# Kernel optimization log

Hardware: AMD Instinct MI355X
Metric: run time of the kernel (lower is better)

Reference implementation:

```python
import jax, jax.numpy as jnp
import numpy as np

B, S, L, Q = 128, 200, 50, 20   # batch, story sentences, sentence len, query len
V, D, K = 50000, 128, 3          # vocab, embed dim, n_hops


def _pe(J, d):
    # position encoding l_kj = (1 - j/J) - (k/d)(1 - 2j/J), 1-indexed
    j = jnp.arange(1, J + 1, dtype=jnp.float32)[:, None]
    k = jnp.arange(1, d + 1, dtype=jnp.float32)[None, :]
    return 1.0 - j / J - (k / d) * (1.0 - 2.0 * j / J)  # (J, d)


def setup_inputs() -> dict:
    key = jax.random.key(0)
    ks = jax.random.split(key, 5)
    story = jax.random.randint(ks[0], (B, S, L), 0, V)
    query = jax.random.randint(ks[1], (B, Q), 0, V)
    # K+1 embedding tables (adjacent weight sharing: A^{k+1} = C^k), sigma=0.1, padding row 0 zeroed
    embs = (jax.random.normal(ks[2], (K + 1, V, D)) * 0.1).at[:, 0, :].set(0.0)
    TA = jax.random.normal(ks[3], (K, S, D)) * 0.1
    TC = jax.random.normal(ks[4], (K, S, D)) * 0.1
    return {"story": story, "query": query, "embs": embs, "TA": TA, "TC": TC}


def reference(story, query, embs, TA, TC):
    d = embs.shape[-1]
    pe_s = _pe(story.shape[-1], d)   # (L, D)
    pe_q = _pe(query.shape[-1], d)   # (Q, D)
    n_hops = TA.shape[0]

    # query embedding with PE: (B, Q, D) * (Q, D) -> sum over Q -> (B, D)
    u = (jnp.take(embs[0], query, axis=0) * pe_q).sum(axis=1)

    for hop in range(n_hops):
        # gather + PE multiply + sum over words + temporal encoding: (B, S, D)
        m = (jnp.take(embs[hop], story, axis=0) * pe_s).sum(axis=2) + TA[hop]
        c = (jnp.take(embs[hop + 1], story, axis=0) * pe_s).sum(axis=2) + TC[hop]
        # attention over memory slots
        p = jax.nn.softmax(jnp.einsum('bsd,bd->bs', m, u), axis=-1)  # (B, S)
        o = jnp.einsum('bs,bsd->bd', p, c)                            # (B, D)
        u = u + o

    # final projection W = embeddings[n_hops].weight -> logits (B, V)
    return u @ embs[n_hops].T
```

## Files before the change

### kernel.cpp

```cpp
#include <hip/hip_runtime.h>

#define B 128
#define S 200
#define LW 50
#define Q 20
#define V 50000
#define D 128
#define NH 3
#define VD (V * D)
#define BSD (B * S * D)
#define BS (B * S)

typedef __bf16 bf16x8 __attribute__((ext_vector_type(8)));
typedef float f32x4 __attribute__((ext_vector_type(4)));
typedef unsigned int u32x4 __attribute__((ext_vector_type(4)));

__device__ __forceinline__ unsigned int f2bf_rne(float f) {
  union { float f; unsigned int u; } c; c.f = f;
  return (c.u + 0x7FFFu + ((c.u >> 16) & 1u)) >> 16;
}
__device__ __forceinline__ unsigned int pack2(float a, float b) {
  return f2bf_rne(a) | (f2bf_rne(b) << 16);
}
__device__ __forceinline__ float bf_lo(unsigned int q) {
  union { unsigned int u; float f; } c; c.u = q << 16; return c.f;
}
__device__ __forceinline__ float bf_hi(unsigned int q) {
  union { unsigned int u; float f; } c; c.u = q & 0xFFFF0000u; return c.f;
}

__global__ __launch_bounds__(256) void k_repack(
    const float* __restrict__ embs, unsigned int* __restrict__ ESM) {
  int v = blockIdx.x * 4 + (threadIdx.x >> 6);
  int l = threadIdx.x & 63;
  int s = l >> 4, c = l & 15;
#pragma unroll
  for (int k = 0; k < 4; ++k) {
    const float2 e = *(const float2*)(embs + (size_t)k * VD + (size_t)v * D + 2 * l);
    ESM[((size_t)(k * 4 + s) * V + v) * 16 + c] = pack2(e.x, e.y);
  }
}

__global__ __launch_bounds__(256) void k_story16(
    const int* __restrict__ story, unsigned short* __restrict__ story16) {
  int i = blockIdx.x * 256 + threadIdx.x;
  int4 v = ((const int4*)story)[i];
  ushort4 o;
  o.x = (unsigned short)v.x; o.y = (unsigned short)v.y;
  o.z = (unsigned short)v.z; o.w = (unsigned short)v.w;
  ((ushort4*)story16)[i] = o;
}

__global__ __launch_bounds__(256) void k_packT(
    const float* __restrict__ TA, const float* __restrict__ TC,
    unsigned int* __restrict__ TAp, unsigned int* __restrict__ TCp) {
  int idx = blockIdx.x * 256 + threadIdx.x;
  int row = idx >> 6;
  int u = idx & 63;
  int d0 = 32 * (u >> 4) + 2 * (u & 15);
  const float2 a = *(const float2*)(TA + (size_t)row * D + d0);
  const float2 c = *(const float2*)(TC + (size_t)row * D + d0);
  TAp[idx] = pack2(a.x, a.y);
  TCp[idx] = pack2(c.x, c.y);
}

__global__ __launch_bounds__(256) void k_gather_slice(
    const unsigned short* __restrict__ story16,
    const u32x4* __restrict__ ESM4, unsigned int* __restrict__ Gp, int phase) {
  __shared__ __align__(16) unsigned short sidx[4][800];
  int unit = blockIdx.x & 7;
  int k = 2 * phase + (unit >> 2);
  int s = unit & 3;
  int widx = blockIdx.x >> 3;
  int w = threadIdx.x >> 6;
  int l = threadIdx.x & 63;
  int g = l >> 2;
  int q = l & 3;
  const u32x4* src4 = ESM4 + (size_t)(k * 4 + s) * V * 4;
  int d0 = s * 32 + 8 * q;
  float kd[8];
#pragma unroll
  for (int i = 0; i < 8; ++i) kd[i] = (float)(d0 + i + 1) * (1.0f / D);

  int sent16 = widx * 64 + w * 16;
  const u32x4* st4 = (const u32x4*)(story16 + sent16 * LW);
  u32x4* dst4 = (u32x4*)sidx[w];
#pragma unroll
  for (int m = 0; m < 2; ++m) {
    int e = l + m * 64;
    if (e < 100) dst4[e] = __builtin_nontemporal_load(st4 + e);
  }
  const unsigned short* wrow = sidx[w] + g * LW;
  float SA[8] = {0.f, 0.f, 0.f, 0.f, 0.f, 0.f, 0.f, 0.f};
  float SB[8] = {0.f, 0.f, 0.f, 0.f, 0.f, 0.f, 0.f, 0.f};
#pragma unroll 10
  for (int j = 0; j < LW; ++j) {
    int idx = (int)wrow[j];
    u32x4 qv = src4[(size_t)idx * 4 + q];
    float jj = (float)(j + 1) * (1.0f / LW);
    float al = 1.0f - jj;
    float bl = 2.0f * jj - 1.0f;
    float ee[8];
    ee[0] = bf_lo(qv.x); ee[1] = bf_hi(qv.x);
    ee[2] = bf_lo(qv.y); ee[3] = bf_hi(qv.y);
    ee[4] = bf_lo(qv.z); ee[5] = bf_hi(qv.z);
    ee[6] = bf_lo(qv.w); ee[7] = bf_hi(qv.w);
#pragma unroll
    for (int i = 0; i < 8; ++i) { SA[i] += ee[i] * al; SB[i] += ee[i] * bl; }
  }
  int sent = sent16 + g;
  u32x4 og;
  og.x = pack2(SA[0] + kd[0] * SB[0], SA[1] + kd[1] * SB[1]);
  og.y = pack2(SA[2] + kd[2] * SB[2], SA[3] + kd[3] * SB[3]);
  og.z = pack2(SA[4] + kd[4] * SB[4], SA[5] + kd[5] * SB[5]);
  og.w = pack2(SA[6] + kd[6] * SB[6], SA[7] + kd[7] * SB[7]);
  __builtin_nontemporal_store(
      og, (u32x4*)(Gp + ((size_t)k * BS + sent) * 64 + s * 16) + q);
}

__global__ __launch_bounds__(1024) void k_hops(
    const unsigned int* __restrict__ G, const unsigned int* __restrict__ TAp,
    const unsigned int* __restrict__ TCp, const int* __restrict__ query,
    const float* __restrict__ emb0, unsigned int* __restrict__ ubf) {
  __shared__ float su[D];
  __shared__ float sp[S];
  __shared__ float sred[2];
  __shared__ float4 oacc[32][32];
  int b = blockIdx.x;
  int t = threadIdx.x;
  if (t < D) {
    float kd = (float)(t + 1) * (1.0f / D);
    float acc = 0.f;
    for (int q = 0; q < Q; ++q) {
      int idx = query[b * Q + q];
      float jj = (float)(q + 1) * (1.0f / Q);
      float pe = 1.0f - jj - kd * (1.0f - 2.0f * jj);
      acc += emb0[(size_t)idx * D + t] * pe;
    }
    su[t] = acc;
  }
  __syncthreads();
  for (int hop = 0; hop < NH; ++hop) {
    const unsigned int* Gm = G + ((size_t)hop * BS + (size_t)b * S) * 64;
    const unsigned int* Gc = G + ((size_t)(hop + 1) * BS + (size_t)b * S) * 64;
    const unsigned int* ta = TAp + (size_t)hop * S * 64;
    const unsigned int* tc = TCp + (size_t)hop * S * 64;
    if (t < 4 * S) {
      int sl = t >> 2, p = t & 3;
      const uint2* gr = (const uint2*)(Gm + (size_t)sl * 64 + p * 16);
      const uint2* tr = (const uint2*)(ta + (size_t)sl * 64 + p * 16);
      float sc = 0.f;
#pragma unroll
      for (int i = 0; i < 8; ++i) {
        uint2 g2 = gr[i];
        uint2 t2 = tr[i];
        int dd = p * 32 + 4 * i;
        sc += (bf_lo(g2.x) + bf_lo(t2.x)) * su[dd + 0];
        sc += (bf_hi(g2.x) + bf_hi(t2.x)) * su[dd + 1];
        sc += (bf_lo(g2.y) + bf_lo(t2.y)) * su[dd + 2];
        sc += (bf_hi(g2.y) + bf_hi(t2.y)) * su[dd + 3];
      }
      sc += __shfl_xor(sc, 1);
      sc += __shfl_xor(sc, 2);
      if (p == 0) sp[sl] = sc;
    }
    __syncthreads();
    if (t < 64) {
      float mx = -1e30f;
      for (int s = t; s < S; s += 64) mx = fmaxf(mx, sp[s]);
#pragma unroll
      for (int off = 1; off < 64; off <<= 1) mx = fmaxf(mx, __shfl_xor(mx, off));
      float sum = 0.f;
      for (int s = t; s < S; s += 64) sum += expf(sp[s] - mx);
#pragma unroll
      for (int off = 1; off < 64; off <<= 1) sum += __shfl_xor(sum, off);
      if (t == 0) { sred[0] = mx; sred[1] = sum; }
    }
    __syncthreads();
    float mx = sred[0];
    float inv = 1.0f / sred[1];
    if (t < S) sp[t] = expf(sp[t] - mx) * inv;
    __syncthreads();
    {
      int g = t >> 5, c = t & 31;
      float4 o4 = {0.f, 0.f, 0.f, 0.f};
      for (int s = g; s < S; s += 32) {
        float p = sp[s];
        uint2 g2 = *(const uint2*)(Gc + (size_t)s * 64 + 2 * c);
        uint2 t2 = *(const uint2*)(tc + (size_t)s * 64 + 2 * c);
        o4.x += p * (bf_lo(g2.x) + bf_lo(t2.x));
        o4.y += p * (bf_hi(g2.x) + bf_hi(t2.x));
        o4.z += p * (bf_lo(g2.y) + bf_lo(t2.y));
        o4.w += p * (bf_hi(g2.y) + bf_hi(t2.y));
      }
      oacc[g][c] = o4;
    }
    __syncthreads();
    if (t < 32) {
      int d0 = (t >> 3) * 32 + (t & 7) * 4;
      float4 o = oacc[0][t];
#pragma unroll
      for (int g = 1; g < 32; ++g) {
        float4 x = oacc[g][t];
        o.x += x.x; o.y += x.y; o.z += x.z; o.w += x.w;
      }
      su[d0 + 0] += o.x;
      su[d0 + 1] += o.y;
      su[d0 + 2] += o.z;
      su[d0 + 3] += o.w;
    }
    __syncthreads();
  }
  if (t < 64) ubf[b * 64 + t] = pack2(su[2 * t], su[2 * t + 1]);
}

__global__ __launch_bounds__(256) void k_logits_mfma(
    const uint4* __restrict__ ubf,
    const uint4* __restrict__ esm,
    float* __restrict__ out) {
  int wid = threadIdx.x >> 6;
  int l = threadIdx.x & 63;
  int lr = l & 15;
  int lk = l >> 4;
  int vbase = blockIdx.x * 128 + wid * 32;
  uint4 bfrag[2][4];
#pragma unroll
  for (int vs = 0; vs < 2; ++vs) {
    int v = vbase + vs * 16 + lr;
    if (v >= V) v = V - 1;
#pragma unroll
    for (int kk = 0; kk < 4; ++kk)
      bfrag[vs][kk] = esm[((size_t)(12 + kk) * V + v) * 4 + lk];
  }
  f32x4 acc[2][8];
#pragma unroll
  for (int vs = 0; vs < 2; ++vs)
#pragma unroll
    for (int m = 0; m < 8; ++m) {
      f32x4 z = {0.f, 0.f, 0.f, 0.f};
      acc[vs][m] = z;
    }
#pragma unroll
  for (int m = 0; m < 8; ++m) {
    uint4 afrag[4];
#pragma unroll
    for (int kk = 0; kk < 4; ++kk)
      afrag[kk] = ubf[(m * 16 + lr) * 16 + kk * 4 + lk];
#pragma unroll
    for (int vs = 0; vs < 2; ++vs)
#pragma unroll
      for (int kk = 0; kk < 4; ++kk)
        acc[vs][m] = __builtin_amdgcn_mfma_f32_16x16x32_bf16(
            __builtin_bit_cast(bf16x8, afrag[kk]),
            __builtin_bit_cast(bf16x8, bfrag[vs][kk]), acc[vs][m], 0, 0, 0);
  }
#pragma unroll
  for (int vs = 0; vs < 2; ++vs) {
    int v = vbase + vs * 16 + lr;
    if (v < V) {
#pragma unroll
      for (int m = 0; m < 8; ++m)
#pragma unroll
        for (int r = 0; r < 4; ++r)
          out[(size_t)(m * 16 + lk * 4 + r) * V + v] = acc[vs][m][r];
    }
  }
}

__global__ __launch_bounds__(128) void k_gather_query(
    const int* __restrict__ query, const float* __restrict__ embs,
    float* __restrict__ u) {
  int b = blockIdx.x;
  int d = threadIdx.x;
  float kd = (float)(d + 1) / (float)D;
  float acc = 0.f;
  for (int q = 0; q < Q; ++q) {
    int idx = query[b * Q + q];
    float jj = (float)(q + 1) / (float)Q;
    float pe = 1.0f - jj - kd * (1.0f - 2.0f * jj);
    acc += embs[(size_t)idx * D + d] * pe;
  }
  u[b * D + d] = acc;
}

__global__ __launch_bounds__(128) void k_gather_story(
    const int* __restrict__ story, const float* __restrict__ embs,
    float* __restrict__ G) {
  int bs = blockIdx.x;
  int d = threadIdx.x;
  const int* w = story + bs * LW;
  float kd = (float)(d + 1) / (float)D;
  float a0 = 0.f, a1 = 0.f, a2 = 0.f, a3 = 0.f;
  for (int l = 0; l < LW; ++l) {
    int idx = w[l];
    float jj = (float)(l + 1) / (float)LW;
    float pe = 1.0f - jj - kd * (1.0f - 2.0f * jj);
    size_t base = (size_t)idx * D + d;
    a0 += embs[base] * pe;
    a1 += embs[base + (size_t)VD] * pe;
    a2 += embs[base + (size_t)(2 * VD)] * pe;
    a3 += embs[base + (size_t)(3 * VD)] * pe;
  }
  size_t o = (size_t)bs * D + d;
  G[o] = a0;
  G[o + (size_t)BSD] = a1;
  G[o + (size_t)(2 * BSD)] = a2;
  G[o + (size_t)(3 * BSD)] = a3;
}

__global__ __launch_bounds__(256) void k_hops_f32(
    const float* __restrict__ G, const float* __restrict__ TA,
    const float* __restrict__ TC, float* __restrict__ u) {
  __shared__ float su[D];
  __shared__ float sp[S];
  __shared__ float sred[2];
  int b = blockIdx.x;
  int t = threadIdx.x;
  if (t < D) su[t] = u[b * D + t];
  __syncthreads();
  for (int hop = 0; hop < NH; ++hop) {
    const float* Gm = G + (size_t)hop * BSD + (size_t)b * S * D;
    const float* Gc = G + (size_t)(hop + 1) * BSD + (size_t)b * S * D;
    const float* ta = TA + hop * S * D;
    const float* tc = TC + hop * S * D;
    if (t < S) {
      float sc = 0.f;
      for (int d = 0; d < D; ++d) sc += (Gm[t * D + d] + ta[t * D + d]) * su[d];
      sp[t] = sc;
    }
    __syncthreads();
    if (t < 64) {
      float mx = -1e30f;
      for (int s = t; s < S; s += 64) mx = fmaxf(mx, sp[s]);
#pragma unroll
      for (int off = 1; off < 64; off <<= 1) mx = fmaxf(mx, __shfl_xor(mx, off));
      float sum = 0.f;
      for (int s = t; s < S; s += 64) sum += expf(sp[s] - mx);
#pragma unroll
      for (int off = 1; off < 64; off <<= 1) sum += __shfl_xor(sum, off);
      if (t == 0) { sred[0] = mx; sred[1] = sum; }
    }
    __syncthreads();
    float mx = sred[0];
    float inv = 1.0f / sred[1];
    if (t < S) sp[t] = expf(sp[t] - mx) * inv;
    __syncthreads();
    if (t < D) {
      float o = 0.f;
      for (int s = 0; s < S; ++s) o += sp[s] * (Gc[s * D + t] + tc[s * D + t]);
      su[t] += o;
    }
    __syncthreads();
  }
  if (t < D) u[b * D + t] = su[t];
}

__global__ __launch_bounds__(256) void k_logits_f32(
    const float* __restrict__ u, const float* __restrict__ e3,
    float* __restrict__ out) {
  __shared__ float sE[64][129];
  __shared__ float sU[64][129];
  int v0 = blockIdx.x * 64;
  int b0 = blockIdx.y * 64;
  int t = threadIdx.x;
  for (int i = 0; i < 32; ++i) {
    int lin = i * 256 + t;
    int r = lin >> 7, c = lin & 127;
    int v = v0 + r;
    sE[r][c] = (v < V) ? e3[(size_t)v * D + c] : 0.f;
    sU[r][c] = u[(b0 + r) * D + c];
  }
  __syncthreads();
  int tv = (t & 15) * 4;
  int tb = (t >> 4) * 4;
  float acc[4][4] = {};
  for (int d = 0; d < D; ++d) {
    float ev[4], ub[4];
#pragma unroll
    for (int i = 0; i < 4; ++i) ev[i] = sE[tv + i][d];
#pragma unroll
    for (int j = 0; j < 4; ++j) ub[j] = sU[tb + j][d];
#pragma unroll
    for (int j = 0; j < 4; ++j)
#pragma unroll
      for (int i = 0; i < 4; ++i) acc[j][i] += ub[j] * ev[i];
  }
  for (int j = 0; j < 4; ++j)
    for (int i = 0; i < 4; ++i) {
      int v = v0 + tv + i;
      if (v < V) out[(size_t)(b0 + tb + j) * V + v] = acc[j][i];
    }
}

extern "C" void kernel_launch(void* const* d_in, const int* in_sizes, int n_in,
                              void* d_out, int out_size, void* d_ws,
                              size_t ws_size, hipStream_t stream) {
  (void)in_sizes; (void)n_in; (void)out_size;
  const int* story = (const int*)d_in[0];
  const int* query = (const int*)d_in[1];
  const float* embs = (const float*)d_in[2];
  const float* TA = (const float*)d_in[3];
  const float* TC = (const float*)d_in[4];
  float* out = (float*)d_out;

  const size_t esm_bytes = (size_t)16 * V * 16 * 4;
  const size_t g_bytes = (size_t)4 * BS * 64 * 4;
  const size_t ub_bytes = (size_t)B * 64 * 4;
  const size_t s16_bytes = (size_t)BS * LW * 2;
  const size_t tp_bytes = (size_t)NH * S * 64 * 4;

  if (ws_size >= esm_bytes + g_bytes + ub_bytes + s16_bytes + 2 * tp_bytes) {
    char* p = (char*)d_ws;
    unsigned int* ESM = (unsigned int*)p;      p += esm_bytes;
    unsigned int* Gp = (unsigned int*)p;       p += g_bytes;
    unsigned int* ubf = (unsigned int*)p;      p += ub_bytes;
    unsigned short* story16 = (unsigned short*)p;  p += s16_bytes;
    unsigned int* TAp = (unsigned int*)p;      p += tp_bytes;
    unsigned int* TCp = (unsigned int*)p;

    k_repack<<<V / 4, 256, 0, stream>>>(embs, ESM);
    k_story16<<<BS * LW / 4 / 256, 256, 0, stream>>>(story, story16);
    k_packT<<<NH * S * 64 / 256, 256, 0, stream>>>(TA, TC, TAp, TCp);
    k_gather_slice<<<3200, 256, 0, stream>>>(story16, (const u32x4*)ESM, Gp, 0);
    k_gather_slice<<<3200, 256, 0, stream>>>(story16, (const u32x4*)ESM, Gp, 1);
    k_hops<<<B, 1024, 0, stream>>>(Gp, TAp, TCp, query, embs, ubf);
    k_logits_mfma<<<(V + 127) / 128, 256, 0, stream>>>(
        (const uint4*)ubf, (const uint4*)ESM, out);
  } else {
    float* G = (float*)d_ws;
    float* u = G + 4 * (size_t)BSD;
    k_gather_query<<<B, D, 0, stream>>>(query, embs, u);
    k_gather_story<<<B * S, D, 0, stream>>>(story, embs, G);
    k_hops_f32<<<B, 256, 0, stream>>>(G, TA, TC, u);
    k_logits_f32<<<dim3((V + 63) / 64, B / 64), 256, 0, stream>>>(
        u, embs + 3 * (size_t)VD, out);
  }
}
```

Before: 171.0 us.

## Split vocab into halves with compacted story indices for cache-resident gathers

Result: slower. 238.4 us (+39.4%).

```diff
diff --git a/kernel.cpp b/kernel.cpp
--- a/kernel.cpp
+++ b/kernel.cpp
@@ -5,6 +5,7 @@
 #define LW 50
 #define Q 20
 #define V 50000
+#define VH 25000
 #define D 128
 #define NH 3
 #define VD (V * D)
@@ -13,6 +14,7 @@
 
 typedef __bf16 bf16x8 __attribute__((ext_vector_type(8)));
 typedef float f32x4 __attribute__((ext_vector_type(4)));
+typedef float f32x2 __attribute__((ext_vector_type(2)));
 typedef unsigned int u32x4 __attribute__((ext_vector_type(4)));
 
 __device__ __forceinline__ unsigned int f2bf_rne(float f) {
@@ -29,26 +31,43 @@
   union { unsigned int u; float f; } c; c.u = q & 0xFFFF0000u; return c.f;
 }
 
-__global__ __launch_bounds__(256) void k_repack(
-    const float* __restrict__ embs, unsigned int* __restrict__ ESM) {
+__global__ __launch_bounds__(256) void k_compact(
+    const int* __restrict__ story, unsigned int* __restrict__ CS,
+    int* __restrict__ cnts) {
+  int sent = blockIdx.x * 256 + threadIdx.x;
+  const int* w = story + sent * LW;
+  unsigned int* row0 = CS + ((size_t)0 * BS + sent) * LW;
+  unsigned int* row1 = CS + ((size_t)1 * BS + sent) * LW;
+  int c0 = 0, c1 = 0;
+  for (int j = 0; j < LW; ++j) {
+    unsigned int idx = (unsigned int)w[j];
+    unsigned int e = idx | ((unsigned int)j << 16);
+    if (idx < (unsigned int)VH) row0[c0++] = e;
+    else row1[c1++] = e;
+  }
+  for (int s = c0; s < LW; ++s) row0[s] = 0u;
+  for (int s = c1; s < LW; ++s) row1[s] = (unsigned int)VH;
+  cnts[0 * BS + sent] = c0;
+  cnts[1 * BS + sent] = c1;
+}
+
+__global__ __launch_bounds__(256) void k_repack_w(
+    const float* __restrict__ embs, unsigned int* __restrict__ ESMW,
+    int kbase) {
   int v = blockIdx.x * 4 + (threadIdx.x >> 6);
   int l = threadIdx.x & 63;
-  int s = l >> 4, c = l & 15;
-#pragma unroll
-  for (int k = 0; k < 4; ++k) {
-    const float2 e = *(const float2*)(embs + (size_t)k * VD + (size_t)v * D + 2 * l);
-    ESM[((size_t)(k * 4 + s) * V + v) * 16 + c] = pack2(e.x, e.y);
-  }
-}
-
-__global__ __launch_bounds__(256) void k_story16(
-    const int* __restrict__ story, unsigned short* __restrict__ story16) {
-  int i = blockIdx.x * 256 + threadIdx.x;
-  int4 v = ((const int4*)story)[i];
-  ushort4 o;
-  o.x = (unsigned short)v.x; o.y = (unsigned short)v.y;
-  o.z = (unsigned short)v.z; o.w = (unsigned short)v.w;
-  ((ushort4*)story16)[i] = o;
+  int dh = l >> 5, cc = l & 31;
+  int h = (v >= VH) ? 1 : 0;
+  int vp = v - h * VH;
+#pragma unroll
+  for (int t = 0; t < 2; ++t) {
+    int k = kbase + t;
+    f32x2 e = __builtin_nontemporal_load(
+        (const f32x2*)(embs + (size_t)k * VD + (size_t)v * D + 2 * l));
+    int r = (t * 2 + dh) * 2 + h;
+    __builtin_nontemporal_store(
+        pack2(e.x, e.y), ESMW + ((size_t)r * VH + vp) * 32 + cc);
+  }
 }
 
 __global__ __launch_bounds__(256) void k_packT(
@@ -57,69 +76,89 @@
   int idx = blockIdx.x * 256 + threadIdx.x;
   int row = idx >> 6;
   int u = idx & 63;
-  int d0 = 32 * (u >> 4) + 2 * (u & 15);
-  const float2 a = *(const float2*)(TA + (size_t)row * D + d0);
-  const float2 c = *(const float2*)(TC + (size_t)row * D + d0);
+  const float2 a = *(const float2*)(TA + (size_t)row * D + 2 * u);
+  const float2 c = *(const float2*)(TC + (size_t)row * D + 2 * u);
   TAp[idx] = pack2(a.x, a.y);
   TCp[idx] = pack2(c.x, c.y);
 }
 
-__global__ __launch_bounds__(256) void k_gather_slice(
-    const unsigned short* __restrict__ story16,
-    const u32x4* __restrict__ ESM4, unsigned int* __restrict__ Gp, int phase) {
-  __shared__ __align__(16) unsigned short sidx[4][800];
-  int unit = blockIdx.x & 7;
-  int k = 2 * phase + (unit >> 2);
-  int s = unit & 3;
-  int widx = blockIdx.x >> 3;
-  int w = threadIdx.x >> 6;
-  int l = threadIdx.x & 63;
-  int g = l >> 2;
-  int q = l & 3;
-  const u32x4* src4 = ESM4 + (size_t)(k * 4 + s) * V * 4;
-  int d0 = s * 32 + 8 * q;
-  float kd[8];
-#pragma unroll
-  for (int i = 0; i < 8; ++i) kd[i] = (float)(d0 + i + 1) * (1.0f / D);
-
-  int sent16 = widx * 64 + w * 16;
-  const u32x4* st4 = (const u32x4*)(story16 + sent16 * LW);
-  u32x4* dst4 = (u32x4*)sidx[w];
-#pragma unroll
-  for (int m = 0; m < 2; ++m) {
-    int e = l + m * 64;
-    if (e < 100) dst4[e] = __builtin_nontemporal_load(st4 + e);
-  }
-  const unsigned short* wrow = sidx[w] + g * LW;
+__global__ __launch_bounds__(256) void k_gather_h(
+    const unsigned int* __restrict__ CS, const int* __restrict__ cnts,
+    const u32x4* __restrict__ ESMW4, unsigned int* __restrict__ Pp,
+    int phase) {
+  __shared__ unsigned int sent_ent[32 * LW];
+  __shared__ int scnt[32];
+  int r = blockIdx.x & 7;
+  int h = r & 1;
+  int dh = (r >> 1) & 1;
+  int t = r >> 2;
+  int ktab = 2 * phase + t;
+  int s0 = (blockIdx.x >> 3) * 32;
+  int tid = threadIdx.x;
+  const unsigned int* src = CS + ((size_t)h * BS + s0) * LW;
+  for (int e = tid; e < 32 * LW; e += 256)
+    sent_ent[e] = __builtin_nontemporal_load(src + e);
+  if (tid < 32) scnt[tid] = cnts[h * BS + s0 + tid];
+  __syncthreads();
+
+  int w = tid >> 6, l = tid & 63;
+  int ss = l >> 3, q8 = l & 7;
+  int sl = w * 8 + ss;
+  int cnt = scnt[sl];
+  int wmax = cnt;
+  wmax = max(wmax, __shfl_xor(wmax, 8));
+  wmax = max(wmax, __shfl_xor(wmax, 16));
+  wmax = max(wmax, __shfl_xor(wmax, 32));
+  const u32x4* reg = ESMW4 + (size_t)r * VH * 8;
+  const unsigned int* ent = sent_ent + sl * LW;
   float SA[8] = {0.f, 0.f, 0.f, 0.f, 0.f, 0.f, 0.f, 0.f};
   float SB[8] = {0.f, 0.f, 0.f, 0.f, 0.f, 0.f, 0.f, 0.f};
-#pragma unroll 10
-  for (int j = 0; j < LW; ++j) {
-    int idx = (int)wrow[j];
-    u32x4 qv = src4[(size_t)idx * 4 + q];
-    float jj = (float)(j + 1) * (1.0f / LW);
-    float al = 1.0f - jj;
-    float bl = 2.0f * jj - 1.0f;
-    float ee[8];
-    ee[0] = bf_lo(qv.x); ee[1] = bf_hi(qv.x);
-    ee[2] = bf_lo(qv.y); ee[3] = bf_hi(qv.y);
-    ee[4] = bf_lo(qv.z); ee[5] = bf_hi(qv.z);
-    ee[6] = bf_lo(qv.w); ee[7] = bf_hi(qv.w);
-#pragma unroll
-    for (int i = 0; i < 8; ++i) { SA[i] += ee[i] * al; SB[i] += ee[i] * bl; }
-  }
-  int sent = sent16 + g;
+  unsigned int hoff = (unsigned int)(h * VH);
+  for (int j = 0; j < wmax; j += 2) {
+    unsigned int e0 = ent[j];
+    unsigned int e1 = ent[j + 1];
+    unsigned int vp0 = (e0 & 0xFFFFu) - hoff;
+    unsigned int vp1 = (e1 & 0xFFFFu) - hoff;
+    u32x4 q0 = reg[(size_t)vp0 * 8 + q8];
+    u32x4 q1 = reg[(size_t)vp1 * 8 + q8];
+    float jj0 = (float)((e0 >> 16) + 1) * (1.0f / LW);
+    float jj1 = (float)((e1 >> 16) + 1) * (1.0f / LW);
+    bool a0 = (j < cnt), a1 = (j + 1 < cnt);
+    float al0 = a0 ? (1.0f - jj0) : 0.f;
+    float bl0 = a0 ? (2.0f * jj0 - 1.0f) : 0.f;
+    float al1 = a1 ? (1.0f - jj1) : 0.f;
+    float bl1 = a1 ? (2.0f * jj1 - 1.0f) : 0.f;
+    float e0f[8], e1f[8];
+    e0f[0] = bf_lo(q0.x); e0f[1] = bf_hi(q0.x);
+    e0f[2] = bf_lo(q0.y); e0f[3] = bf_hi(q0.y);
+    e0f[4] = bf_lo(q0.z); e0f[5] = bf_hi(q0.z);
+    e0f[6] = bf_lo(q0.w); e0f[7] = bf_hi(q0.w);
+    e1f[0] = bf_lo(q1.x); e1f[1] = bf_hi(q1.x);
+    e1f[2] = bf_lo(q1.y); e1f[3] = bf_hi(q1.y);
+    e1f[4] = bf_lo(q1.z); e1f[5] = bf_hi(q1.z);
+    e1f[6] = bf_lo(q1.w); e1f[7] = bf_hi(q1.w);
+#pragma unroll
+    for (int i = 0; i < 8; ++i) {
+      SA[i] += e0f[i] * al0 + e1f[i] * al1;
+      SB[i] += e0f[i] * bl0 + e1f[i] * bl1;
+    }
+  }
+  int dbase = dh * 64 + q8 * 8;
+  float kd[8];
+#pragma unroll
+  for (int i = 0; i < 8; ++i) kd[i] = (float)(dbase + i + 1) * (1.0f / D);
+  int sent = s0 + sl;
   u32x4 og;
   og.x = pack2(SA[0] + kd[0] * SB[0], SA[1] + kd[1] * SB[1]);
   og.y = pack2(SA[2] + kd[2] * SB[2], SA[3] + kd[3] * SB[3]);
   og.z = pack2(SA[4] + kd[4] * SB[4], SA[5] + kd[5] * SB[5]);
   og.w = pack2(SA[6] + kd[6] * SB[6], SA[7] + kd[7] * SB[7]);
   __builtin_nontemporal_store(
-      og, (u32x4*)(Gp + ((size_t)k * BS + sent) * 64 + s * 16) + q);
+      og, (u32x4*)Pp + (((size_t)(ktab * 2 + h) * BS + sent) * 16 + dh * 8 + q8));
 }
 
 __global__ __launch_bounds__(1024) void k_hops(
-    const unsigned int* __restrict__ G, const unsigned int* __restrict__ TAp,
+    const unsigned int* __restrict__ P, const unsigned int* __restrict__ TAp,
     const unsigned int* __restrict__ TCp, const int* __restrict__ query,
     const float* __restrict__ emb0, unsigned int* __restrict__ ubf) {
   __shared__ float su[D];
@@ -141,24 +180,29 @@
   }
   __syncthreads();
   for (int hop = 0; hop < NH; ++hop) {
-    const unsigned int* Gm = G + ((size_t)hop * BS + (size_t)b * S) * 64;
-    const unsigned int* Gc = G + ((size_t)(hop + 1) * BS + (size_t)b * S) * 64;
+    const unsigned int* m0 = P + ((size_t)(hop * 2 + 0) * BS + (size_t)b * S) * 64;
+    const unsigned int* m1 = P + ((size_t)(hop * 2 + 1) * BS + (size_t)b * S) * 64;
+    const unsigned int* c0 = P + ((size_t)((hop + 1) * 2 + 0) * BS + (size_t)b * S) * 64;
+    const unsigned int* c1 = P + ((size_t)((hop + 1) * 2 + 1) * BS + (size_t)b * S) * 64;
     const unsigned int* ta = TAp + (size_t)hop * S * 64;
     const unsigned int* tc = TCp + (size_t)hop * S * 64;
     if (t < 4 * S) {
       int sl = t >> 2, p = t & 3;
-      const uint2* gr = (const uint2*)(Gm + (size_t)sl * 64 + p * 16);
-      const uint2* tr = (const uint2*)(ta + (size_t)sl * 64 + p * 16);
+      size_t off = (size_t)sl * 64 + p * 16;
+      const uint2* g0 = (const uint2*)(m0 + off);
+      const uint2* g1 = (const uint2*)(m1 + off);
+      const uint2* tr = (const uint2*)(ta + off);
       float sc = 0.f;
 #pragma unroll
       for (int i = 0; i < 8; ++i) {
-        uint2 g2 = gr[i];
+        uint2 a2 = g0[i];
+        uint2 b2 = g1[i];
         uint2 t2 = tr[i];
         int dd = p * 32 + 4 * i;
-        sc += (bf_lo(g2.x) + bf_lo(t2.x)) * su[dd + 0];
-        sc += (bf_hi(g2.x) + bf_hi(t2.x)) * su[dd + 1];
-        sc += (bf_lo(g2.y) + bf_lo(t2.y)) * su[dd + 2];
-        sc += (bf_hi(g2.y) + bf_hi(t2.y)) * su[dd + 3];
+        sc += (bf_lo(a2.x) + bf_lo(b2.x) + bf_lo(t2.x)) * su[dd + 0];
+        sc += (bf_hi(a2.x) + bf_hi(b2.x) + bf_hi(t2.x)) * su[dd + 1];
+        sc += (bf_lo(a2.y) + bf_lo(b2.y) + bf_lo(t2.y)) * su[dd + 2];
+        sc += (bf_hi(a2.y) + bf_hi(b2.y) + bf_hi(t2.y)) * su[dd + 3];
       }
       sc += __shfl_xor(sc, 1);
       sc += __shfl_xor(sc, 2);
@@ -185,19 +229,20 @@
       int g = t >> 5, c = t & 31;
       float4 o4 = {0.f, 0.f, 0.f, 0.f};
       for (int s = g; s < S; s += 32) {
-        float p = sp[s];
-        uint2 g2 = *(const uint2*)(Gc + (size_t)s * 64 + 2 * c);
+        float p5 = sp[s];
+        uint2 a2 = *(const uint2*)(c0 + (size_t)s * 64 + 2 * c);
+        uint2 b2 = *(const uint2*)(c1 + (size_t)s * 64 + 2 * c);
         uint2 t2 = *(const uint2*)(tc + (size_t)s * 64 + 2 * c);
-        o4.x += p * (bf_lo(g2.x) + bf_lo(t2.x));
-        o4.y += p * (bf_hi(g2.x) + bf_hi(t2.x));
-        o4.z += p * (bf_lo(g2.y) + bf_lo(t2.y));
-        o4.w += p * (bf_hi(g2.y) + bf_hi(t2.y));
+        o4.x += p5 * (bf_lo(a2.x) + bf_lo(b2.x) + bf_lo(t2.x));
+        o4.y += p5 * (bf_hi(a2.x) + bf_hi(b2.x) + bf_hi(t2.x));
+        o4.z += p5 * (bf_lo(a2.y) + bf_lo(b2.y) + bf_lo(t2.y));
+        o4.w += p5 * (bf_hi(a2.y) + bf_hi(b2.y) + bf_hi(t2.y));
       }
       oacc[g][c] = o4;
     }
     __syncthreads();
     if (t < 32) {
-      int d0 = (t >> 3) * 32 + (t & 7) * 4;
+      int d0 = 4 * t;
       float4 o = oacc[0][t];
 #pragma unroll
       for (int g = 1; g < 32; ++g) {
@@ -216,36 +261,42 @@
 
 __global__ __launch_bounds__(256) void k_logits_mfma(
     const uint4* __restrict__ ubf,
-    const uint4* __restrict__ esm,
+    const u32x4* __restrict__ esmw4,
     float* __restrict__ out) {
   int wid = threadIdx.x >> 6;
   int l = threadIdx.x & 63;
   int lr = l & 15;
   int lk = l >> 4;
   int vbase = blockIdx.x * 128 + wid * 32;
-  uint4 bfrag[2][4];
+  int mbase = blockIdx.y * 4;
+  u32x4 bfrag[2][4];
 #pragma unroll
   for (int vs = 0; vs < 2; ++vs) {
     int v = vbase + vs * 16 + lr;
     if (v >= V) v = V - 1;
+    int h = (v >= VH) ? 1 : 0;
+    int vp = v - h * VH;
 #pragma unroll
     for (int kk = 0; kk < 4; ++kk)
-      bfrag[vs][kk] = esm[((size_t)(12 + kk) * V + v) * 4 + lk];
-  }
-  f32x4 acc[2][8];
+      bfrag[vs][kk] =
+          esmw4[((size_t)(4 + 2 * (kk >> 1) + h) * VH + vp) * 8 +
+                (kk & 1) * 4 + lk];
+  }
+  f32x4 acc[2][4];
 #pragma unroll
   for (int vs = 0; vs < 2; ++vs)
 #pragma unroll
-    for (int m = 0; m < 8; ++m) {
+    for (int m = 0; m < 4; ++m) {
       f32x4 z = {0.f, 0.f, 0.f, 0.f};
       acc[vs][m] = z;
     }
 #pragma unroll
-  for (int m = 0; m < 8; ++m) {
+  for (int m = 0; m < 4; ++m) {
+    int gm = mbase + m;
     uint4 afrag[4];
 #pragma unroll
     for (int kk = 0; kk < 4; ++kk)
-      afrag[kk] = ubf[(m * 16 + lr) * 16 + kk * 4 + lk];
+      afrag[kk] = ubf[(gm * 16 + lr) * 16 + kk * 4 + lk];
 #pragma unroll
     for (int vs = 0; vs < 2; ++vs)
 #pragma unroll
@@ -259,10 +310,10 @@
     int v = vbase + vs * 16 + lr;
     if (v < V) {
 #pragma unroll
-      for (int m = 0; m < 8; ++m)
+      for (int m = 0; m < 4; ++m)
 #pragma unroll
         for (int r = 0; r < 4; ++r)
-          out[(size_t)(m * 16 + lk * 4 + r) * V + v] = acc[vs][m][r];
+          out[(size_t)((mbase + m) * 16 + lk * 4 + r) * V + v] = acc[vs][m][r];
     }
   }
 }
@@ -403,29 +454,36 @@
   const float* TC = (const float*)d_in[4];
   float* out = (float*)d_out;
 
-  const size_t esm_bytes = (size_t)16 * V * 16 * 4;
-  const size_t g_bytes = (size_t)4 * BS * 64 * 4;
+  const size_t esmw_bytes = (size_t)8 * VH * 128;
+  const size_t pp_bytes = (size_t)8 * BS * 64 * 4;
+  const size_t cs_bytes = (size_t)2 * BS * LW * 4;
+  const size_t cnt_bytes = (size_t)2 * BS * 4;
+  const size_t tp_bytes = (size_t)NH * S * 64 * 4;
   const size_t ub_bytes = (size_t)B * 64 * 4;
-  const size_t s16_bytes = (size_t)BS * LW * 2;
-  const size_t tp_bytes = (size_t)NH * S * 64 * 4;
-
-  if (ws_size >= esm_bytes + g_bytes + ub_bytes + s16_bytes + 2 * tp_bytes) {
+  const size_t need = esmw_bytes + pp_bytes + cs_bytes + cnt_bytes +
+                      2 * tp_bytes + ub_bytes;
+
+  if (ws_size >= need) {
     char* p = (char*)d_ws;
-    unsigned int* ESM = (unsigned int*)p;      p += esm_bytes;
-    unsigned int* Gp = (unsigned int*)p;       p += g_bytes;
-    unsigned int* ubf = (unsigned int*)p;      p += ub_bytes;
-    unsigned short* story16 = (unsigned short*)p;  p += s16_bytes;
-    unsigned int* TAp = (unsigned int*)p;      p += tp_bytes;
-    unsigned int* TCp = (unsigned int*)p;
-
-    k_repack<<<V / 4, 256, 0, stream>>>(embs, ESM);
-    k_story16<<<BS * LW / 4 / 256, 256, 0, stream>>>(story, story16);
+    unsigned int* ESMW = (unsigned int*)p;   p += esmw_bytes;
+    unsigned int* Pp = (unsigned int*)p;     p += pp_bytes;
+    unsigned int* CS = (unsigned int*)p;     p += cs_bytes;
+    int* cnts = (int*)p;                     p += cnt_bytes;
+    unsigned int* TAp = (unsigned int*)p;    p += tp_bytes;
+    unsigned int* TCp = (unsigned int*)p;    p += tp_bytes;
+    unsigned int* ubf = (unsigned int*)p;
+
+    k_compact<<<BS / 256, 256, 0, stream>>>(story, CS, cnts);
     k_packT<<<NH * S * 64 / 256, 256, 0, stream>>>(TA, TC, TAp, TCp);
-    k_gather_slice<<<3200, 256, 0, stream>>>(story16, (const u32x4*)ESM, Gp, 0);
-    k_gather_slice<<<3200, 256, 0, stream>>>(story16, (const u32x4*)ESM, Gp, 1);
-    k_hops<<<B, 1024, 0, stream>>>(Gp, TAp, TCp, query, embs, ubf);
-    k_logits_mfma<<<(V + 127) / 128, 256, 0, stream>>>(
-        (const uint4*)ubf, (const uint4*)ESM, out);
+    k_repack_w<<<V / 4, 256, 0, stream>>>(embs, ESMW, 0);
+    k_gather_h<<<6400, 256, 0, stream>>>(
+        CS, cnts, (const u32x4*)ESMW, Pp, 0);
+    k_repack_w<<<V / 4, 256, 0, stream>>>(embs, ESMW, 2);
+    k_gather_h<<<6400, 256, 0, stream>>>(
+        CS, cnts, (const u32x4*)ESMW, Pp, 1);
+    k_hops<<<B, 1024, 0, stream>>>(Pp, TAp, TCp, query, embs, ubf);
+    k_logits_mfma<<<dim3((V + 127) / 128, 2), 256, 0, stream>>>(
+        (const uint4*)ubf, (const u32x4*)ESMW, out);
   } else {
     float* G = (float*)d_ws;
     float* u = G + 4 * (size_t)BSD;
```
